# Kernel tuning notes

Hardware: AMD Instinct MI355X
Metric: run time of the kernel (lower is better)

## Reference

```python
import jax, jax.numpy as jnp
import numpy as np

HIDDEN = 4096
NUM_HEADS = 32
NUM_KV_HEADS = 8
HEAD_DIM = HIDDEN // NUM_HEADS  # 128
ROPE_THETA = 500000.0
WORLD_SIZE = 4  # number of ring blocks (simulated single-device)


def setup_inputs() -> dict:
    key = jax.random.key(0)
    ks = jax.random.split(key, 5)
    B, S = 1, 2048
    wscale = HIDDEN ** -0.5  # keep activations O(1)
    return {
        "hidden_states": jax.random.normal(ks[0], (B, S, HIDDEN), jnp.float32),
        "position_ids": jnp.broadcast_to(jnp.arange(S, dtype=jnp.int32), (B, S)),
        "q_proj": jax.random.normal(ks[1], (NUM_HEADS * HEAD_DIM, HIDDEN), jnp.float32) * wscale,
        "k_proj": jax.random.normal(ks[2], (NUM_KV_HEADS * HEAD_DIM, HIDDEN), jnp.float32) * wscale,
        "v_proj": jax.random.normal(ks[3], (NUM_KV_HEADS * HEAD_DIM, HIDDEN), jnp.float32) * wscale,
        "o_proj": jax.random.normal(ks[4], (HIDDEN, NUM_HEADS * HEAD_DIM), jnp.float32) * wscale,
    }


def _rope_cos_sin(position_ids):
    # LlamaRotaryEmbedding: inv_freq over even dims, emb = cat(freqs, freqs)
    inv_freq = 1.0 / (ROPE_THETA ** (jnp.arange(0, HEAD_DIM, 2, dtype=jnp.float32) / HEAD_DIM))
    freqs = position_ids.astype(jnp.float32)[..., None] * inv_freq  # [B,S,HD/2]
    emb = jnp.concatenate([freqs, freqs], axis=-1)                  # [B,S,HD]
    return jnp.cos(emb), jnp.sin(emb)


def _rotate_half(x):
    x1, x2 = jnp.split(x, 2, axis=-1)
    return jnp.concatenate([-x2, x1], axis=-1)


def _attention_forward(hidden_states, q_proj, k_proj, v_proj, o_proj, position_ids):
    B, S, _ = hidden_states.shape
    # projections (no bias), layout [B, S, H, D] as in the source (view before RoPE)
    q = (hidden_states @ q_proj.T).reshape(B, S, NUM_HEADS, HEAD_DIM)
    k = (hidden_states @ k_proj.T).reshape(B, S, NUM_KV_HEADS, HEAD_DIM)
    v = (hidden_states @ v_proj.T).reshape(B, S, NUM_KV_HEADS, HEAD_DIM)

    cos, sin = _rope_cos_sin(position_ids)        # [B,S,HD]
    c, s = cos[:, :, None, :], sin[:, :, None, :]  # unsqueeze_dim=2
    q = q * c + _rotate_half(q) * s
    k = k * c + _rotate_half(k) * s

    # GQA: expand KV heads to match query heads
    groups = NUM_HEADS // NUM_KV_HEADS
    k = jnp.repeat(k, groups, axis=2)  # [B,S,NH,HD]
    v = jnp.repeat(v, groups, axis=2)

    sm_scale = HEAD_DIM ** -0.5
    blk = S // WORLD_SIZE

    # ring: per-KV-block partial attention (non-causal, as no mask is passed) + LSE
    outs, lses = [], []
    for w in range(WORLD_SIZE):
        kb = k[:, w * blk:(w + 1) * blk]
        vb = v[:, w * blk:(w + 1) * blk]
        scores = jnp.einsum('bqhd,bkhd->bhqk', q, kb) * sm_scale  # [B,NH,S,blk]
        m = jnp.max(scores, axis=-1, keepdims=True)
        p = jnp.exp(scores - m)
        l = jnp.sum(p, axis=-1, keepdims=True)
        outs.append(jnp.einsum('bhqk,bkhd->bqhd', p / l, vb))      # normalized partial out
        lses.append((m + jnp.log(l))[..., 0])                      # [B,NH,S]

    # merge_attentions: weight each block by exp(lse_b - logsumexp(lse))
    lse_all = jnp.stack(lses, axis=0)                 # [W,B,NH,S]
    wgt = jax.nn.softmax(lse_all, axis=0)
    attn = sum(outs[w] * jnp.transpose(wgt[w], (0, 2, 1))[..., None]
               for w in range(WORLD_SIZE))            # [B,S,NH,HD]

    attn = attn.reshape(B, S, NUM_HEADS * HEAD_DIM)
    return attn @ o_proj.T


def reference(hidden_states, position_ids, q_proj, k_proj, v_proj, o_proj):
    return _attention_forward(hidden_states, q_proj, k_proj, v_proj, o_proj, position_ids)
```

## Files before the change

### kernel.cpp

```cpp
#include <hip/hip_runtime.h>
#include <stdint.h>
#include <cmath>

typedef unsigned short u16;
typedef unsigned int u32;
typedef __attribute__((ext_vector_type(8))) __bf16 bf16x8;
typedef __attribute__((ext_vector_type(4))) float f32x4;

#define HIDDEN 4096
#define NH 32
#define NKV 8
#define HD 128
#define S_LEN 2048

__device__ __forceinline__ u16 f2bf(float f) {
    u32 x = __float_as_uint(f);
    x += 0x7fff + ((x >> 16) & 1);
    return (u16)(x >> 16);
}
__device__ __forceinline__ float bf2f(u16 u) {
    return __uint_as_float(((u32)u) << 16);
}
__device__ __forceinline__ float fexp2(float x) {
#if __has_builtin(__builtin_amdgcn_exp2f)
    return __builtin_amdgcn_exp2f(x);
#else
    return __expf(x * 0.6931471805599453f);
#endif
}

typedef __attribute__((address_space(1))) const void gv_t;
typedef __attribute__((address_space(3))) void lv_t;
__device__ __forceinline__ void async16(const u16* g, u16* s) {
    __builtin_amdgcn_global_load_lds((gv_t*)g, (lv_t*)s, 16, 0, 0);
}

__global__ void cvt_bf16(const float* __restrict__ src, u16* __restrict__ dst, int n4) {
    int i = blockIdx.x * 256 + threadIdx.x;
    if (i < n4) {
        float4 v = ((const float4*)src)[i];
        union { u16 u[4]; uint2 w; } pk;
        pk.u[0] = f2bf(v.x); pk.u[1] = f2bf(v.y);
        pk.u[2] = f2bf(v.z); pk.u[3] = f2bf(v.w);
        ((uint2*)dst)[i] = pk.w;
    }
}

#define GEMM_PROLOGUE_AND_MAINLOOP(Aptr, Bptr, Kdim)                                   \
    __shared__ u16 sA[128 * 64];                                                       \
    __shared__ u16 sB[128 * 64];                                                       \
    const int tid = threadIdx.x;                                                       \
    const int w = tid >> 6, lane = tid & 63;                                           \
    const int l15 = lane & 15, quad = lane >> 4;                                       \
    const int m0 = blockIdx.y * 128, n0 = blockIdx.x * 128;                            \
    const int wm = w & 1, wn = w >> 1;                                                 \
    f32x4 acc[4][4];                                                                   \
    _Pragma("unroll") for (int mi = 0; mi < 4; ++mi)                                   \
    _Pragma("unroll") for (int ni = 0; ni < 4; ++ni)                                   \
    _Pragma("unroll") for (int r = 0; r < 4; ++r) acc[mi][ni][r] = 0.f;                \
    for (int kt = 0; kt < (Kdim); kt += 64) {                                          \
        _Pragma("unroll") for (int i = 0; i < 4; ++i) {                                \
            int c = (i * 4 + w) * 64 + lane;                                           \
            int r = c >> 3, sl = c & 7, g = sl ^ (r & 7);                              \
            async16((Aptr) + (size_t)(m0 + r) * (Kdim) + kt + g * 8, &sA[c * 8]);      \
        }                                                                              \
        _Pragma("unroll") for (int i = 0; i < 4; ++i) {                                \
            int c = (i * 4 + w) * 64 + lane;                                           \
            int r = c >> 3, sl = c & 7, g = sl ^ (r & 7);                              \
            async16((Bptr) + (size_t)(n0 + r) * (Kdim) + kt + g * 8, &sB[c * 8]);      \
        }                                                                              \
        __syncthreads();                                                               \
        _Pragma("unroll") for (int ks = 0; ks < 2; ++ks) {                             \
            bf16x8 af[4], bf[4];                                                       \
            _Pragma("unroll") for (int t = 0; t < 4; ++t) {                            \
                int row = wm * 64 + t * 16 + l15;                                      \
                int sl = (ks * 4 + quad) ^ (row & 7);                                  \
                af[t] = *(const bf16x8*)&sA[row * 64 + sl * 8];                        \
            }                                                                          \
            _Pragma("unroll") for (int t = 0; t < 4; ++t) {                            \
                int row = wn * 64 + t * 16 + l15;                                      \
                int sl = (ks * 4 + quad) ^ (row & 7);                                  \
                bf[t] = *(const bf16x8*)&sB[row * 64 + sl * 8];                        \
            }                                                                          \
            _Pragma("unroll") for (int mi = 0; mi < 4; ++mi)                           \
            _Pragma("unroll") for (int ni = 0; ni < 4; ++ni)                           \
                acc[mi][ni] = __builtin_amdgcn_mfma_f32_16x16x32_bf16(                 \
                    af[mi], bf[ni], acc[mi][ni], 0, 0, 0);                             \
        }                                                                              \
        __syncthreads();                                                               \
    }

__global__ __launch_bounds__(256, 2) void gemm_bt_f32(
    const u16* __restrict__ A, const u16* __restrict__ B, float* __restrict__ C,
    int N, int K)
{
    GEMM_PROLOGUE_AND_MAINLOOP(A, B, K)
#pragma unroll
    for (int mi = 0; mi < 4; ++mi) {
        int row = m0 + wm * 64 + mi * 16 + quad * 4;
#pragma unroll
        for (int ni = 0; ni < 4; ++ni) {
            int col = n0 + wn * 64 + ni * 16 + l15;
#pragma unroll
            for (int r = 0; r < 4; ++r)
                C[(size_t)(row + r) * N + col] = acc[mi][ni][r];
        }
    }
}

__global__ __launch_bounds__(256, 2) void gemm_qkv(
    const u16* __restrict__ A, const u16* __restrict__ B,
    u16* __restrict__ qb, u16* __restrict__ kbuf, u16* __restrict__ vt)
{
    GEMM_PROLOGUE_AND_MAINLOOP(A, B, HIDDEN)
    if (n0 < 4096 + 1024) {
        u16* outp; int ldo, cb;
        if (n0 < 4096) { outp = qb; ldo = HIDDEN; cb = n0; }
        else           { outp = kbuf; ldo = NKV * HD; cb = n0 - 4096; }
#pragma unroll
        for (int mi = 0; mi < 4; ++mi) {
            int row = m0 + wm * 64 + mi * 16 + quad * 4;
#pragma unroll
            for (int ni = 0; ni < 4; ++ni) {
                int col = cb + wn * 64 + ni * 16 + l15;
#pragma unroll
                for (int r = 0; r < 4; ++r)
                    outp[(size_t)(row + r) * ldo + col] = f2bf(acc[mi][ni][r]);
            }
        }
    } else {
        int cb = n0 - (4096 + 1024);
#pragma unroll
        for (int mi = 0; mi < 4; ++mi) {
            int row = m0 + wm * 64 + mi * 16 + quad * 4;
#pragma unroll
            for (int ni = 0; ni < 4; ++ni) {
                int c = cb + wn * 64 + ni * 16 + l15;
                union { u16 u[4]; uint2 v; } pk;
#pragma unroll
                for (int r = 0; r < 4; ++r) pk.u[r] = f2bf(acc[mi][ni][r]);
                *(uint2*)&vt[(size_t)c * S_LEN + row] = pk.v;
            }
        }
    }
}

struct DTab { double f[64]; };
__global__ void rope_k(u16* __restrict__ buf, const int* __restrict__ pos,
                       int logH, int total, float oscale, DTab tab)
{
    int idx = blockIdx.x * 256 + threadIdx.x;
    if (idx >= total) return;
    int d = idx & 63;
    int rest = idx >> 6;
    int s = rest >> logH;
    double fr = (double)pos[s] * tab.f[d];
    double sd, cd;
    sincos(fr, &sd, &cd);
    float c = (float)cd * oscale, sn = (float)sd * oscale;
    u16* p = buf + (size_t)rest * HD + d;
    float x1 = bf2f(p[0]), x2 = bf2f(p[64]);
    p[0]  = f2bf(x1 * c - x2 * sn);
    p[64] = f2bf(x2 * c + x1 * sn);
}

__global__ __launch_bounds__(512, 1) void attn_kernel(
    const u16* __restrict__ Q, const u16* __restrict__ Kb,
    const u16* __restrict__ Vt, u16* __restrict__ O)
{
    __shared__ u16 sK[128 * 128];
    __shared__ u16 sV[128 * 128];
    __shared__ __align__(16) u16 sP[8][16 * 264];
    __shared__ float sAl[8][32];

    const int tid = threadIdx.x;
    const int w = tid >> 6, lane = tid & 63;
    const int l15 = lane & 15, quad = lane >> 4;
    const int h = blockIdx.y, q0 = blockIdx.x * 256;
    const int hk = h >> 2;
    u16* const sPw = sP[w];

    bf16x8 qf[2][4];
#pragma unroll
    for (int mt = 0; mt < 2; ++mt)
#pragma unroll
        for (int ks = 0; ks < 4; ++ks)
            qf[mt][ks] = *(const bf16x8*)(Q + (size_t)(q0 + w * 32 + mt * 16 + l15) * HIDDEN
                                           + h * HD + ks * 32 + quad * 8);

    f32x4 oc[8][2];
#pragma unroll
    for (int dt = 0; dt < 8; ++dt)
#pragma unroll
        for (int nt = 0; nt < 2; ++nt)
#pragma unroll
            for (int r = 0; r < 4; ++r) oc[dt][nt][r] = 0.f;
    float m_r[2][4], l_r[2][4];
#pragma unroll
    for (int mt = 0; mt < 2; ++mt)
#pragma unroll
        for (int r = 0; r < 4; ++r) { m_r[mt][r] = -1e30f; l_r[mt][r] = 0.f; }

    for (int kbi = 0; kbi < 16; ++kbi) {
        const int k0 = kbi * 128;

#pragma unroll
        for (int i = 0; i < 4; ++i) {
            int c = i * 512 + tid;
            int r = c >> 4, sl = c & 15, g = sl ^ (r & 15);
            async16(Kb + (size_t)(k0 + r) * (NKV * HD) + hk * HD + g * 8, &sK[c * 8]);
        }
#pragma unroll
        for (int i = 0; i < 4; ++i) {
            int c = i * 512 + tid;
            int r = c >> 4, sl = c & 15, g = sl ^ (r & 15);
            async16(Vt + (size_t)(hk * HD + r) * S_LEN + k0 + g * 8, &sV[c * 8]);
        }
        __syncthreads();

        f32x4 sa[2][8];
#pragma unroll
        for (int mt = 0; mt < 2; ++mt)
#pragma unroll
            for (int nt = 0; nt < 8; ++nt)
#pragma unroll
                for (int r = 0; r < 4; ++r) sa[mt][nt][r] = 0.f;
#pragma unroll
        for (int ks = 0; ks < 4; ++ks) {
            bf16x8 kf[8];
#pragma unroll
            for (int nt = 0; nt < 8; ++nt) {
                int row = nt * 16 + l15;
                int sl = (ks * 4 + quad) ^ (row & 15);
                kf[nt] = *(const bf16x8*)&sK[row * 128 + sl * 8];
            }
#pragma unroll
            for (int mt = 0; mt < 2; ++mt)
#pragma unroll
                for (int nt = 0; nt < 8; ++nt)
                    sa[mt][nt] = __builtin_amdgcn_mfma_f32_16x16x32_bf16(
                        qf[mt][ks], kf[nt], sa[mt][nt], 0, 0, 0);
        }

#pragma unroll
        for (int mt = 0; mt < 2; ++mt)
#pragma unroll
            for (int r = 0; r < 4; ++r) {
                float mx = sa[mt][0][r];
#pragma unroll
                for (int nt = 1; nt < 8; ++nt) mx = fmaxf(mx, sa[mt][nt][r]);
#pragma unroll
                for (int off = 1; off < 16; off <<= 1)
                    mx = fmaxf(mx, __shfl_xor(mx, off, 16));
                float mnew = fmaxf(m_r[mt][r], mx);
                float alpha = fexp2(m_r[mt][r] - mnew);
                m_r[mt][r] = mnew;
                int ql = mt * 16 + quad * 4 + r;
                u16* pb = sPw + (l15 >> 3) * 264 + ql * 8 + (l15 & 7);
                float rs = 0.f;
#pragma unroll
                for (int nt = 0; nt < 8; ++nt) {
                    float p = fexp2(sa[mt][nt][r] - mnew);
                    rs += p;
                    pb[nt * 528] = f2bf(p);
                }
#pragma unroll
                for (int off = 1; off < 16; off <<= 1)
                    rs += __shfl_xor(rs, off, 16);
                l_r[mt][r] = l_r[mt][r] * alpha + rs;
                if (l15 == 0) sAl[w][ql] = alpha;
            }

        float al0 = sAl[w][l15], al1 = sAl[w][16 + l15];
#pragma unroll
        for (int dt = 0; dt < 8; ++dt)
#pragma unroll
            for (int r = 0; r < 4; ++r) { oc[dt][0][r] *= al0; oc[dt][1][r] *= al1; }

#pragma unroll
        for (int ks = 0; ks < 4; ++ks) {
            bf16x8 vf[8], pf[2];
#pragma unroll
            for (int dt = 0; dt < 8; ++dt) {
                int row = dt * 16 + l15;
                int sl = (ks * 4 + quad) ^ (row & 15);
                vf[dt] = *(const bf16x8*)&sV[row * 128 + sl * 8];
            }
#pragma unroll
            for (int nt = 0; nt < 2; ++nt)
                pf[nt] = *(const bf16x8*)&sPw[(ks * 4 + quad) * 264 + (nt * 16 + l15) * 8];
#pragma unroll
            for (int dt = 0; dt < 8; ++dt)
#pragma unroll
                for (int nt = 0; nt < 2; ++nt)
                    oc[dt][nt] = __builtin_amdgcn_mfma_f32_16x16x32_bf16(
                        vf[dt], pf[nt], oc[dt][nt], 0, 0, 0);
        }

        __syncthreads();
    }

#pragma unroll
    for (int mt = 0; mt < 2; ++mt)
#pragma unroll
        for (int r = 0; r < 4; ++r)
            if (l15 == 0) sAl[w][mt * 16 + quad * 4 + r] = l_r[mt][r];
    float il[2];
    il[0] = 1.f / sAl[w][l15];
    il[1] = 1.f / sAl[w][16 + l15];
#pragma unroll
    for (int nt = 0; nt < 2; ++nt)
#pragma unroll
        for (int dt = 0; dt < 8; ++dt) {
            union { u16 u[4]; uint2 v; } pk;
#pragma unroll
            for (int r = 0; r < 4; ++r) pk.u[r] = f2bf(oc[dt][nt][r] * il[nt]);
            *(uint2*)(O + (size_t)(q0 + w * 32 + nt * 16 + l15) * HIDDEN
                        + h * HD + dt * 16 + quad * 4) = pk.v;
        }
}

extern "C" void kernel_launch(void* const* d_in, const int* in_sizes, int n_in,
                              void* d_out, int out_size, void* d_ws, size_t ws_size,
                              hipStream_t stream) {
    const float* hs = (const float*)d_in[0];
    const int* pos  = (const int*)d_in[1];
    const float* wq = (const float*)d_in[2];
    const float* wk = (const float*)d_in[3];
    const float* wv = (const float*)d_in[4];
    const float* wo = (const float*)d_in[5];
    float* out = (float*)d_out;

    u16* ws    = (u16*)d_ws;
    u16* hid16 = ws;
    u16* wq16  = hid16 + (size_t)S_LEN * HIDDEN;
    u16* wk16  = wq16 + (size_t)HIDDEN * HIDDEN;
    u16* wv16  = wk16 + (size_t)NKV * HD * HIDDEN;
    u16* wo16  = wv16 + (size_t)NKV * HD * HIDDEN;
    u16* qb    = wo16 + (size_t)HIDDEN * HIDDEN;
    u16* kb    = qb + (size_t)S_LEN * HIDDEN;
    u16* vt    = kb + (size_t)S_LEN * NKV * HD;
    u16* at    = vt + (size_t)S_LEN * NKV * HD;

    dim3 blk(256);
    auto cvt = [&](const float* s, u16* d, size_t n) {
        int n4 = (int)(n / 4);
        cvt_bf16<<<dim3((n4 + 255) / 256), blk, 0, stream>>>(s, d, n4);
    };
    cvt(hs, hid16, (size_t)S_LEN * HIDDEN);
    cvt(wq, wq16, (size_t)HIDDEN * HIDDEN);
    cvt(wk, wk16, (size_t)NKV * HD * HIDDEN);
    cvt(wv, wv16, (size_t)NKV * HD * HIDDEN);
    cvt(wo, wo16, (size_t)HIDDEN * HIDDEN);

    gemm_qkv<<<dim3((HIDDEN + 2 * NKV * HD) / 128, S_LEN / 128), blk, 0, stream>>>(
        hid16, wq16, qb, kb, vt);

    DTab tab;
    for (int i = 0; i < 64; ++i) tab.f[i] = pow(500000.0, -(double)i / 64.0);
    const float qscale = 0.08838834764831845f * 1.4426950408889634f;
    rope_k<<<dim3(S_LEN * NH * 64 / 256), blk, 0, stream>>>(
        qb, pos, 5, S_LEN * NH * 64, qscale, tab);
    rope_k<<<dim3(S_LEN * NKV * 64 / 256), blk, 0, stream>>>(
        kb, pos, 3, S_LEN * NKV * 64, 1.0f, tab);

    attn_kernel<<<dim3(S_LEN / 256, NH), dim3(512), 0, stream>>>(qb, kb, vt, at);

    gemm_bt_f32<<<dim3(HIDDEN / 128, S_LEN / 128), blk, 0, stream>>>(
        at, wo16, out, HIDDEN, HIDDEN);
}
```

Baseline: 545.3 us.

## Prefetch K/V tiles in attention, DPP reductions, fuse convert and RoPE launches

The attention loop now issues the async load of the next K tile right after the softmax and the next V tile right after the PV MMA, each behind a barrier, so global-to-LDS loads overlap compute instead of stalling at the top of every iteration. The 16-lane shuffle reductions for row max and sum are replaced with DPP row-rotate operations. The five fp32-to-bf16 conversion launches are merged into one kernel. RoPE now builds a per-position cos/sin table once in double precision and applies it to Q and K in a single launch, instead of recomputing double sincos for every head. The cost is an extra barrier per attention iteration and an extra workspace buffer for the table.

```diff
diff --git a/kernel.cpp b/kernel.cpp
--- a/kernel.cpp
+++ b/kernel.cpp
@@ -29,21 +29,51 @@
 #endif
 }
 
+template <int N>
+__device__ __forceinline__ float dpp_ror(float v) {
+    int i = __builtin_amdgcn_update_dpp(0, __float_as_int(v),
+                                        0x120 + N, 0xf, 0xf, true);
+    return __int_as_float(i);
+}
+__device__ __forceinline__ float row_max16(float x) {
+    x = fmaxf(x, dpp_ror<1>(x));
+    x = fmaxf(x, dpp_ror<2>(x));
+    x = fmaxf(x, dpp_ror<4>(x));
+    x = fmaxf(x, dpp_ror<8>(x));
+    return x;
+}
+__device__ __forceinline__ float row_sum16(float x) {
+    x += dpp_ror<1>(x);
+    x += dpp_ror<2>(x);
+    x += dpp_ror<4>(x);
+    x += dpp_ror<8>(x);
+    return x;
+}
+
 typedef __attribute__((address_space(1))) const void gv_t;
 typedef __attribute__((address_space(3))) void lv_t;
 __device__ __forceinline__ void async16(const u16* g, u16* s) {
     __builtin_amdgcn_global_load_lds((gv_t*)g, (lv_t*)s, 16, 0, 0);
 }
 
-__global__ void cvt_bf16(const float* __restrict__ src, u16* __restrict__ dst, int n4) {
-    int i = blockIdx.x * 256 + threadIdx.x;
-    if (i < n4) {
-        float4 v = ((const float4*)src)[i];
-        union { u16 u[4]; uint2 w; } pk;
-        pk.u[0] = f2bf(v.x); pk.u[1] = f2bf(v.y);
-        pk.u[2] = f2bf(v.z); pk.u[3] = f2bf(v.w);
-        ((uint2*)dst)[i] = pk.w;
-    }
+#define F4_HS   2097152u
+#define F4_WQ   4194304u
+#define F4_WKV  1048576u
+__global__ void cvt_all(const float* __restrict__ s0, const float* __restrict__ s1,
+                        const float* __restrict__ s2, const float* __restrict__ s3,
+                        const float* __restrict__ s4, u16* __restrict__ dst) {
+    u32 i = blockIdx.x * 256 + threadIdx.x;
+    const float* src; u32 off;
+    if (i < F4_HS)                              { src = s0; off = 0; }
+    else if (i < F4_HS + F4_WQ)                 { src = s1; off = F4_HS; }
+    else if (i < F4_HS + F4_WQ + F4_WKV)        { src = s2; off = F4_HS + F4_WQ; }
+    else if (i < F4_HS + F4_WQ + 2 * F4_WKV)    { src = s3; off = F4_HS + F4_WQ + F4_WKV; }
+    else                                        { src = s4; off = F4_HS + F4_WQ + 2 * F4_WKV; }
+    float4 v = ((const float4*)src)[i - off];
+    union { u16 u[4]; uint2 w; } pk;
+    pk.u[0] = f2bf(v.x); pk.u[1] = f2bf(v.y);
+    pk.u[2] = f2bf(v.z); pk.u[3] = f2bf(v.w);
+    ((uint2*)dst)[i] = pk.w;
 }
 
 #define GEMM_PROLOGUE_AND_MAINLOOP(Aptr, Bptr, Kdim)                                   \
@@ -146,18 +176,28 @@
 }
 
 struct DTab { double f[64]; };
-__global__ void rope_k(u16* __restrict__ buf, const int* __restrict__ pos,
-                       int logH, int total, float oscale, DTab tab)
-{
+__global__ void rope_table(const int* __restrict__ pos, float2* __restrict__ tab,
+                           DTab dt) {
     int idx = blockIdx.x * 256 + threadIdx.x;
-    if (idx >= total) return;
+    int d = idx & 63, s = idx >> 6;
+    double fr = (double)pos[s] * dt.f[d];
+    double sd, cd;
+    sincos(fr, &sd, &cd);
+    tab[idx] = make_float2((float)cd, (float)sd);
+}
+
+#define Q_ITEMS (S_LEN * NH * 64)
+__global__ void rope_apply(u16* __restrict__ qb, u16* __restrict__ kb,
+                           const float2* __restrict__ tab, float qscale) {
+    int idx = blockIdx.x * 256 + threadIdx.x;
+    u16* buf; int logH; float osc;
+    if (idx < Q_ITEMS) { buf = qb; logH = 5; osc = qscale; }
+    else { idx -= Q_ITEMS; buf = kb; logH = 3; osc = 1.0f; }
     int d = idx & 63;
     int rest = idx >> 6;
     int s = rest >> logH;
-    double fr = (double)pos[s] * tab.f[d];
-    double sd, cd;
-    sincos(fr, &sd, &cd);
-    float c = (float)cd * oscale, sn = (float)sd * oscale;
+    float2 cs = tab[s * 64 + d];
+    float c = cs.x * osc, sn = cs.y * osc;
     u16* p = buf + (size_t)rest * HD + d;
     float x1 = bf2f(p[0]), x2 = bf2f(p[64]);
     p[0]  = f2bf(x1 * c - x2 * sn);
@@ -201,23 +241,28 @@
 #pragma unroll
         for (int r = 0; r < 4; ++r) { m_r[mt][r] = -1e30f; l_r[mt][r] = 0.f; }
 
-    for (int kbi = 0; kbi < 16; ++kbi) {
-        const int k0 = kbi * 128;
-
+    auto stageK = [&](int k0) {
 #pragma unroll
         for (int i = 0; i < 4; ++i) {
             int c = i * 512 + tid;
             int r = c >> 4, sl = c & 15, g = sl ^ (r & 15);
             async16(Kb + (size_t)(k0 + r) * (NKV * HD) + hk * HD + g * 8, &sK[c * 8]);
         }
+    };
+    auto stageV = [&](int k0) {
 #pragma unroll
         for (int i = 0; i < 4; ++i) {
             int c = i * 512 + tid;
             int r = c >> 4, sl = c & 15, g = sl ^ (r & 15);
             async16(Vt + (size_t)(hk * HD + r) * S_LEN + k0 + g * 8, &sV[c * 8]);
         }
-        __syncthreads();
-
+    };
+
+    stageK(0);
+    stageV(0);
+    __syncthreads();
+
+    for (int kbi = 0; kbi < 16; ++kbi) {
         f32x4 sa[2][8];
 #pragma unroll
         for (int mt = 0; mt < 2; ++mt)
@@ -249,9 +294,7 @@
                 float mx = sa[mt][0][r];
 #pragma unroll
                 for (int nt = 1; nt < 8; ++nt) mx = fmaxf(mx, sa[mt][nt][r]);
-#pragma unroll
-                for (int off = 1; off < 16; off <<= 1)
-                    mx = fmaxf(mx, __shfl_xor(mx, off, 16));
+                mx = row_max16(mx);
                 float mnew = fmaxf(m_r[mt][r], mx);
                 float alpha = fexp2(m_r[mt][r] - mnew);
                 m_r[mt][r] = mnew;
@@ -264,12 +307,13 @@
                     rs += p;
                     pb[nt * 528] = f2bf(p);
                 }
-#pragma unroll
-                for (int off = 1; off < 16; off <<= 1)
-                    rs += __shfl_xor(rs, off, 16);
+                rs = row_sum16(rs);
                 l_r[mt][r] = l_r[mt][r] * alpha + rs;
                 if (l15 == 0) sAl[w][ql] = alpha;
             }
+
+        __syncthreads();
+        if (kbi < 15) stageK((kbi + 1) * 128);
 
         float al0 = sAl[w][l15], al1 = sAl[w][16 + l15];
 #pragma unroll
@@ -298,6 +342,7 @@
         }
 
         __syncthreads();
+        if (kbi < 15) stageV((kbi + 1) * 128);
     }
 
 #pragma unroll
@@ -341,28 +386,21 @@
     u16* kb    = qb + (size_t)S_LEN * HIDDEN;
     u16* vt    = kb + (size_t)S_LEN * NKV * HD;
     u16* at    = vt + (size_t)S_LEN * NKV * HD;
+    float2* tab = (float2*)(at + (size_t)S_LEN * HIDDEN);
 
     dim3 blk(256);
-    auto cvt = [&](const float* s, u16* d, size_t n) {
-        int n4 = (int)(n / 4);
-        cvt_bf16<<<dim3((n4 + 255) / 256), blk, 0, stream>>>(s, d, n4);
-    };
-    cvt(hs, hid16, (size_t)S_LEN * HIDDEN);
-    cvt(wq, wq16, (size_t)HIDDEN * HIDDEN);
-    cvt(wk, wk16, (size_t)NKV * HD * HIDDEN);
-    cvt(wv, wv16, (size_t)NKV * HD * HIDDEN);
-    cvt(wo, wo16, (size_t)HIDDEN * HIDDEN);
+
+    cvt_all<<<dim3(12582912u / 256), blk, 0, stream>>>(hs, wq, wk, wv, wo, hid16);
 
     gemm_qkv<<<dim3((HIDDEN + 2 * NKV * HD) / 128, S_LEN / 128), blk, 0, stream>>>(
         hid16, wq16, qb, kb, vt);
 
-    DTab tab;
-    for (int i = 0; i < 64; ++i) tab.f[i] = pow(500000.0, -(double)i / 64.0);
+    DTab dt;
+    for (int i = 0; i < 64; ++i) dt.f[i] = pow(500000.0, -(double)i / 64.0);
     const float qscale = 0.08838834764831845f * 1.4426950408889634f;
-    rope_k<<<dim3(S_LEN * NH * 64 / 256), blk, 0, stream>>>(
-        qb, pos, 5, S_LEN * NH * 64, qscale, tab);
-    rope_k<<<dim3(S_LEN * NKV * 64 / 256), blk, 0, stream>>>(
-        kb, pos, 3, S_LEN * NKV * 64, 1.0f, tab);
+    rope_table<<<dim3(S_LEN * 64 / 256), blk, 0, stream>>>(pos, tab, dt);
+    rope_apply<<<dim3((Q_ITEMS + S_LEN * NKV * 64) / 256), blk, 0, stream>>>(
+        qb, kb, tab, qscale);
 
     attn_kernel<<<dim3(S_LEN / 256, NH), dim3(512), 0, stream>>>(qb, kb, vt, at);
 
```

Measured after the change: 519.3 us. -4.8%, faster.
